# Optimization experiments

Hardware: AMD Instinct MI355X
Metric: run time of the kernel (lower is better)

Reference implementation:

```python
import jax, jax.numpy as jnp
import numpy as np

N = 100000       # nodes
E0 = 1600000     # random edges (self-loops appended -> E = E0 + N)
IN = 128         # input feature dim
H1, C1 = 8, 8    # conv1 heads, out channels per head
C2 = 64          # num_classes (conv2 out, heads=1)
NEG_SLOPE = 0.2


def gat_conv(x, src, dst, W, att_src, att_dst, bias, heads, out_ch, concat):
    """PyG-style GATConv (eval mode, no dropout). x: [N, F_in]."""
    n = x.shape[0]
    h = (x @ W).reshape(n, heads, out_ch)              # [N, H, C]
    a_src = jnp.sum(h * att_src, axis=-1)              # [N, H]
    a_dst = jnp.sum(h * att_dst, axis=-1)              # [N, H]
    e = jax.nn.leaky_relu(a_src[src] + a_dst[dst], NEG_SLOPE)  # [E, H]
    # segment softmax over edges grouped by destination node
    e_max = jax.ops.segment_max(e, dst, num_segments=n)
    ex = jnp.exp(e - e_max[dst])
    denom = jax.ops.segment_sum(ex, dst, num_segments=n)
    alpha = ex / denom[dst]                            # [E, H]
    msg = h[src] * alpha[:, :, None]                   # [E, H, C]
    out = jax.ops.segment_sum(msg, dst, num_segments=n)  # [N, H, C]
    out = out.reshape(n, heads * out_ch) if concat else out.mean(axis=1)
    return out + bias


def setup_inputs() -> dict:
    key = jax.random.key(0)
    ks = jax.random.split(key, 12)
    nodes = jnp.arange(N, dtype=jnp.int32)
    feat = jax.random.normal(ks[0], (N, IN), jnp.float32)
    src = jax.random.randint(ks[1], (E0,), 0, N, jnp.int32)
    dst = jax.random.randint(ks[2], (E0,), 0, N, jnp.int32)
    loop = jnp.arange(N, dtype=jnp.int32)
    edge_index = jnp.stack([jnp.concatenate([src, loop]),
                            jnp.concatenate([dst, loop])])  # [2, E]
    mask = jnp.ones((N,), bool)
    label = jax.random.randint(ks[3], (N,), 0, C2, jnp.int32)
    s = 0.1
    W1 = jax.random.normal(ks[4], (IN, H1 * C1), jnp.float32) * s
    att_src1 = jax.random.normal(ks[5], (H1, C1), jnp.float32) * s
    att_dst1 = jax.random.normal(ks[6], (H1, C1), jnp.float32) * s
    b1 = jnp.zeros((H1 * C1,), jnp.float32)
    W2 = jax.random.normal(ks[7], (H1 * C1, C2), jnp.float32) * s
    att_src2 = jax.random.normal(ks[8], (1, C2), jnp.float32) * s
    att_dst2 = jax.random.normal(ks[9], (1, C2), jnp.float32) * s
    b2 = jnp.zeros((C2,), jnp.float32)
    return {"nodes": nodes, "feat": feat, "edge_index": edge_index, "mask": mask,
            "label": label, "W1": W1, "att_src1": att_src1, "att_dst1": att_dst1,
            "b1": b1, "W2": W2, "att_src2": att_src2, "att_dst2": att_dst2, "b2": b2}


def reference(nodes, feat, edge_index, mask, label,
              W1, att_src1, att_dst1, b1, W2, att_src2, att_dst2, b2):
    src, dst = edge_index[0], edge_index[1]
    x = jax.nn.elu(gat_conv(feat, src, dst, W1, att_src1, att_dst1, b1,
                            H1, C1, concat=True))          # [N, 64]
    scores = gat_conv(x, src, dst, W2, att_src2, att_dst2, b2,
                      1, C2, concat=False)                  # [N, C2]
    logp = jax.nn.log_softmax(scores, axis=-1)
    nll = -jnp.take_along_axis(logp, label[:, None].astype(jnp.int32), axis=1)[:, 0]
    m = mask.astype(scores.dtype)
    loss = jnp.sum(nll * m) / jnp.sum(m)                    # masked mean CE
    pred = jnp.argmax(scores, axis=1)
    return loss, pred, label
```

## Files before the change

### kernel.cpp

```cpp
#include <hip/hip_runtime.h>
#include <cstdint>

#define NHEAD 8
#define D1 64
#define IN_F 128
#define NEG 0.2f
#define NBINS 256
#define BINS 1024
#define BSH 7
#define CHUNK 8192

__device__ __forceinline__ void fma4(float4& a, float s, const float4& v)
{
    a.x = fmaf(s, v.x, a.x); a.y = fmaf(s, v.y, a.y);
    a.z = fmaf(s, v.z, a.z); a.w = fmaf(s, v.w, a.w);
}

__global__ __launch_bounds__(256) void k_gemm1_hist(
    const float* __restrict__ feat,
    const float* __restrict__ W1,
    const float* __restrict__ att_s,
    const float* __restrict__ att_d,
    float* __restrict__ h1, float* __restrict__ a_src, float* __restrict__ a_dst,
    const int* __restrict__ dst, int* __restrict__ btot, int* __restrict__ bh,
    int N, int E, int GH)
{
    __shared__ float Wh[32 * 64];
    __shared__ float Fh[64 * 36];
    const int tid = threadIdx.x;

    if ((int)blockIdx.x < GH) {
        int* hist = (int*)Wh;
        for (int b = tid; b < BINS; b += 256) hist[b] = 0;
        __syncthreads();
        const int e0 = blockIdx.x * CHUNK;
        #pragma unroll
        for (int r = 0; r < 8; ++r) {
            int e = e0 + r * 1024 + tid * 4;
            if (e + 3 < E) {
                int4 d4 = *(const int4*)&dst[e];
                atomicAdd(&hist[d4.x >> BSH], 1);
                atomicAdd(&hist[d4.y >> BSH], 1);
                atomicAdd(&hist[d4.z >> BSH], 1);
                atomicAdd(&hist[d4.w >> BSH], 1);
            } else {
                for (int k = e; k < E && k < e + 4; ++k)
                    atomicAdd(&hist[dst[k] >> BSH], 1);
            }
        }
        __syncthreads();
        for (int b = tid; b < BINS; b += 256) {
            int c = hist[b];
            bh[(size_t)blockIdx.x * BINS + b] = c;
            if (c) atomicAdd(&btot[b * 16], c);
        }
        return;
    }

    const int tx = tid & 15, ty = tid >> 4;
    const int base = (blockIdx.x - GH) * 64;
    float4 acc0 = {0,0,0,0}, acc1 = {0,0,0,0}, acc2 = {0,0,0,0}, acc3 = {0,0,0,0};

    for (int p = 0; p < 4; ++p) {
        if (p) __syncthreads();
        for (int i = tid; i < 32 * 64; i += 256)
            Wh[i] = W1[p * 2048 + i];
        for (int i = tid; i < 64 * 32; i += 256) {
            int r = i >> 5, kk = i & 31;
            int n = base + r;
            Fh[r * 36 + kk] = (n < N) ? feat[(size_t)n * IN_F + p * 32 + kk] : 0.f;
        }
        __syncthreads();
        const float* wk = &Wh[4 * tx];
        const float* f0 = &Fh[(4 * ty + 0) * 36];
        const float* f1 = &Fh[(4 * ty + 1) * 36];
        const float* f2 = &Fh[(4 * ty + 2) * 36];
        const float* f3 = &Fh[(4 * ty + 3) * 36];
        #pragma unroll
        for (int kk = 0; kk < 32; kk += 4) {
            float4 fa = *(const float4*)&f0[kk];
            float4 fb = *(const float4*)&f1[kk];
            float4 fc = *(const float4*)&f2[kk];
            float4 fd = *(const float4*)&f3[kk];
            float4 w0 = *(const float4*)&wk[(kk + 0) * 64];
            float4 w1 = *(const float4*)&wk[(kk + 1) * 64];
            float4 w2 = *(const float4*)&wk[(kk + 2) * 64];
            float4 w3 = *(const float4*)&wk[(kk + 3) * 64];
            fma4(acc0, fa.x, w0); fma4(acc0, fa.y, w1); fma4(acc0, fa.z, w2); fma4(acc0, fa.w, w3);
            fma4(acc1, fb.x, w0); fma4(acc1, fb.y, w1); fma4(acc1, fb.z, w2); fma4(acc1, fb.w, w3);
            fma4(acc2, fc.x, w0); fma4(acc2, fc.y, w1); fma4(acc2, fc.z, w2); fma4(acc2, fc.w, w3);
            fma4(acc3, fd.x, w0); fma4(acc3, fd.y, w1); fma4(acc3, fd.z, w2); fma4(acc3, fd.w, w3);
        }
    }
    const float4 as4 = *(const float4*)&att_s[4 * tx];
    const float4 ad4 = *(const float4*)&att_d[4 * tx];
    float4 accs[4] = {acc0, acc1, acc2, acc3};
    #pragma unroll
    for (int i = 0; i < 4; ++i) {
        int n = base + 4 * ty + i;
        if (n < N) {
            *(float4*)&h1[(size_t)n * D1 + 4 * tx] = accs[i];
            float ps = accs[i].x * as4.x + accs[i].y * as4.y + accs[i].z * as4.z + accs[i].w * as4.w;
            float pd = accs[i].x * ad4.x + accs[i].y * ad4.y + accs[i].z * ad4.z + accs[i].w * ad4.w;
            ps += __shfl_xor(ps, 1);
            pd += __shfl_xor(pd, 1);
            if ((tx & 1) == 0) {
                a_src[n * NHEAD + (tx >> 1)] = ps;
                a_dst[n * NHEAD + (tx >> 1)] = pd;
            }
        }
    }
}

__device__ __forceinline__ int block_incl_scan(int v, int tid, int* lds4)
{
    int lane = tid & 63, w = tid >> 6;
    #pragma unroll
    for (int off = 1; off < 64; off <<= 1) {
        int t = __shfl_up(v, off);
        if (lane >= off) v += t;
    }
    if (lane == 63) lds4[w] = v;
    __syncthreads();
    int add = 0;
    #pragma unroll
    for (int i = 0; i < 4; ++i)
        if (i < w) add += lds4[i];
    __syncthreads();
    return v + add;
}

__global__ __launch_bounds__(256) void k_bscan(
    const int* __restrict__ btot, int* __restrict__ bbase, int* __restrict__ gcur,
    double* __restrict__ bins)
{
    __shared__ int lds4[4];
    const int tid = threadIdx.x;
    bins[tid] = 0.0;
    int c0 = btot[(4 * tid + 0) * 16];
    int c1 = btot[(4 * tid + 1) * 16];
    int c2 = btot[(4 * tid + 2) * 16];
    int c3 = btot[(4 * tid + 3) * 16];
    int v = c0 + c1 + c2 + c3;
    int incl = block_incl_scan(v, tid, lds4);
    int b0 = incl - v, b1 = b0 + c0, b2 = b1 + c1, b3 = b2 + c2;
    bbase[4 * tid + 0] = b0; gcur[(4 * tid + 0) * 16] = b0;
    bbase[4 * tid + 1] = b1; gcur[(4 * tid + 1) * 16] = b1;
    bbase[4 * tid + 2] = b2; gcur[(4 * tid + 2) * 16] = b2;
    bbase[4 * tid + 3] = b3; gcur[(4 * tid + 3) * 16] = b3;
}

__global__ __launch_bounds__(256) void k_scatter(
    const int* __restrict__ src, const int* __restrict__ dst,
    const int* __restrict__ bh, int* __restrict__ gcur,
    int* __restrict__ bucketed, int E)
{
    __shared__ int base[BINS], cur[BINS];
    const int tid = threadIdx.x;
    for (int b = tid; b < BINS; b += 256) {
        cur[b] = 0;
        int c = bh[(size_t)blockIdx.x * BINS + b];
        if (c) base[b] = atomicAdd(&gcur[b * 16], c);
    }
    __syncthreads();
    const int e0 = blockIdx.x * CHUNK;
    #pragma unroll
    for (int r = 0; r < 8; ++r) {
        int e = e0 + r * 1024 + tid * 4;
        if (e + 3 < E) {
            int4 d4 = *(const int4*)&dst[e];
            int4 s4 = *(const int4*)&src[e];
            int bx, rx;
            bx = d4.x >> BSH; rx = atomicAdd(&cur[bx], 1); bucketed[base[bx] + rx] = ((d4.x & 127) << 17) | s4.x;
            bx = d4.y >> BSH; rx = atomicAdd(&cur[bx], 1); bucketed[base[bx] + rx] = ((d4.y & 127) << 17) | s4.y;
            bx = d4.z >> BSH; rx = atomicAdd(&cur[bx], 1); bucketed[base[bx] + rx] = ((d4.z & 127) << 17) | s4.z;
            bx = d4.w >> BSH; rx = atomicAdd(&cur[bx], 1); bucketed[base[bx] + rx] = ((d4.w & 127) << 17) | s4.w;
        } else {
            for (int k = e; k < E && k < e + 4; ++k) {
                int d = dst[k];
                int bx = d >> BSH;
                int rx = atomicAdd(&cur[bx], 1);
                bucketed[base[bx] + rx] = ((d & 127) << 17) | src[k];
            }
        }
    }
}

__global__ __launch_bounds__(256) void k_seg(
    const int* __restrict__ btot, const int* __restrict__ bbase,
    const int* __restrict__ bucketed,
    int* __restrict__ deg, int* __restrict__ rowstart, int* __restrict__ srcs, int N)
{
    __shared__ int cnt[128], cur[128], lb[128];
    const int tid = threadIdx.x;
    const int b = blockIdx.x;
    const int gs = bbase[b];
    const int sz = btot[b * 16];
    if (tid < 128) { cnt[tid] = 0; cur[tid] = 0; }
    __syncthreads();
    for (int i = tid; i < sz; i += 256)
        atomicAdd(&cnt[bucketed[gs + i] >> 17], 1);
    __syncthreads();
    if (tid < 128) lb[tid] = cnt[tid];
    __syncthreads();
    #pragma unroll
    for (int off = 1; off < 128; off <<= 1) {
        int t = 0;
        if (tid < 128 && tid >= off) t = lb[tid - off];
        __syncthreads();
        if (tid < 128 && tid >= off) lb[tid] += t;
        __syncthreads();
    }
    if (tid < 128) {
        int ex = lb[tid] - cnt[tid];
        lb[tid] = ex;
        int d = b * 128 + tid;
        if (d < N) { deg[d] = cnt[tid]; rowstart[d] = gs + ex; }
    }
    __syncthreads();
    for (int i = tid; i < sz; i += 256) {
        int v = bucketed[gs + i];
        int d7 = v >> 17;
        int r = atomicAdd(&cur[d7], 1);
        srcs[gs + lb[d7] + r] = v & 0x1FFFF;
    }
}

__global__ __launch_bounds__(256) void k_agg1(
    const int* __restrict__ deg, const int* __restrict__ rowstart,
    const int* __restrict__ srcs,
    const float* __restrict__ a_s, const float* __restrict__ a_d,
    const float* __restrict__ h1, const float* __restrict__ b1,
    float* __restrict__ x, int N)
{
    const int tid = threadIdx.x, w = tid >> 6, j = tid & 63;
    const int t = j & 15, q = j >> 4;
    const int n = blockIdx.x * 4 + w;
    if (n >= N) return;
    const int rlen = deg[n];
    const int row = rowstart[n];
    const int h = t >> 1;
    const float ad = a_d[n * NHEAD + h];
    float4 acc = {0.f, 0.f, 0.f, 0.f};
    float den = 0.f;
    for (int base = 0; base < rlen; base += 16) {
        int mTot = rlen - base;
        if (4 * q < mTot) {
            int rem = mTot - 4 * q;
            int i0 = row + base + 4 * q;
            int s0 = srcs[i0];
            int s1 = rem > 1 ? srcs[i0 + 1] : 0;
            int s2 = rem > 2 ? srcs[i0 + 2] : 0;
            int s3 = rem > 3 ? srcs[i0 + 3] : 0;
            float v0 = a_s[s0 * NHEAD + h] + ad;
            float v1 = a_s[s1 * NHEAD + h] + ad;
            float v2 = a_s[s2 * NHEAD + h] + ad;
            float v3 = a_s[s3 * NHEAD + h] + ad;
            v0 = v0 > 0.f ? v0 : NEG * v0;
            v1 = v1 > 0.f ? v1 : NEG * v1;
            v2 = v2 > 0.f ? v2 : NEG * v2;
            v3 = v3 > 0.f ? v3 : NEG * v3;
            float e0 = __expf(v0);
            float e1 = rem > 1 ? __expf(v1) : 0.f;
            float e2 = rem > 2 ? __expf(v2) : 0.f;
            float e3 = rem > 3 ? __expf(v3) : 0.f;
            float4 l0 = *(const float4*)&h1[(size_t)s0 * D1 + 4 * t];
            float4 l1 = *(const float4*)&h1[(size_t)s1 * D1 + 4 * t];
            float4 l2 = *(const float4*)&h1[(size_t)s2 * D1 + 4 * t];
            float4 l3 = *(const float4*)&h1[(size_t)s3 * D1 + 4 * t];
            fma4(acc, e0, l0); fma4(acc, e1, l1);
            fma4(acc, e2, l2); fma4(acc, e3, l3);
            den += (e0 + e1) + (e2 + e3);
        }
    }
    acc.x += __shfl_xor(acc.x, 16); acc.y += __shfl_xor(acc.y, 16);
    acc.z += __shfl_xor(acc.z, 16); acc.w += __shfl_xor(acc.w, 16);
    den   += __shfl_xor(den, 16);
    acc.x += __shfl_xor(acc.x, 32); acc.y += __shfl_xor(acc.y, 32);
    acc.z += __shfl_xor(acc.z, 32); acc.w += __shfl_xor(acc.w, 32);
    den   += __shfl_xor(den, 32);
    if (q == 0) {
        float4 b = *(const float4*)&b1[4 * t];
        float4 o;
        o.x = acc.x / den + b.x; o.y = acc.y / den + b.y;
        o.z = acc.z / den + b.z; o.w = acc.w / den + b.w;
        o.x = o.x > 0.f ? o.x : expm1f(o.x);
        o.y = o.y > 0.f ? o.y : expm1f(o.y);
        o.z = o.z > 0.f ? o.z : expm1f(o.z);
        o.w = o.w > 0.f ? o.w : expm1f(o.w);
        *(float4*)&x[(size_t)n * D1 + 4 * t] = o;
    }
}

__global__ __launch_bounds__(256) void k_gemm2(
    const float* __restrict__ x,
    const float* __restrict__ W2,
    const float* __restrict__ att_s,
    const float* __restrict__ att_d,
    float* __restrict__ h2, float* __restrict__ a_src, float* __restrict__ a_dst,
    int N)
{
    __shared__ float Wh[64 * 64];
    __shared__ float Fh[64 * 68];
    const int tid = threadIdx.x;
    const int tx = tid & 15, ty = tid >> 4;
    const int base = blockIdx.x * 64;
    for (int i = tid; i < 64 * 64; i += 256)
        Wh[i] = W2[i];
    for (int i = tid; i < 64 * 64; i += 256) {
        int r = i >> 6, kk = i & 63;
        int n = base + r;
        Fh[r * 68 + kk] = (n < N) ? x[(size_t)n * 64 + kk] : 0.f;
    }
    __syncthreads();
    float4 acc0 = {0,0,0,0}, acc1 = {0,0,0,0}, acc2 = {0,0,0,0}, acc3 = {0,0,0,0};
    const float* wk = &Wh[4 * tx];
    const float* f0 = &Fh[(4 * ty + 0) * 68];
    const float* f1 = &Fh[(4 * ty + 1) * 68];
    const float* f2 = &Fh[(4 * ty + 2) * 68];
    const float* f3 = &Fh[(4 * ty + 3) * 68];
    #pragma unroll 4
    for (int kk = 0; kk < 64; kk += 4) {
        float4 fa = *(const float4*)&f0[kk];
        float4 fb = *(const float4*)&f1[kk];
        float4 fc = *(const float4*)&f2[kk];
        float4 fd = *(const float4*)&f3[kk];
        float4 w0 = *(const float4*)&wk[(kk + 0) * 64];
        float4 w1 = *(const float4*)&wk[(kk + 1) * 64];
        float4 w2 = *(const float4*)&wk[(kk + 2) * 64];
        float4 w3 = *(const float4*)&wk[(kk + 3) * 64];
        fma4(acc0, fa.x, w0); fma4(acc0, fa.y, w1); fma4(acc0, fa.z, w2); fma4(acc0, fa.w, w3);
        fma4(acc1, fb.x, w0); fma4(acc1, fb.y, w1); fma4(acc1, fb.z, w2); fma4(acc1, fb.w, w3);
        fma4(acc2, fc.x, w0); fma4(acc2, fc.y, w1); fma4(acc2, fc.z, w2); fma4(acc2, fc.w, w3);
        fma4(acc3, fd.x, w0); fma4(acc3, fd.y, w1); fma4(acc3, fd.z, w2); fma4(acc3, fd.w, w3);
    }
    const float4 as4 = *(const float4*)&att_s[4 * tx];
    const float4 ad4 = *(const float4*)&att_d[4 * tx];
    float4 accs[4] = {acc0, acc1, acc2, acc3};
    #pragma unroll
    for (int i = 0; i < 4; ++i) {
        int n = base + 4 * ty + i;
        if (n < N) {
            *(float4*)&h2[(size_t)n * 64 + 4 * tx] = accs[i];
            float ps = accs[i].x * as4.x + accs[i].y * as4.y + accs[i].z * as4.z + accs[i].w * as4.w;
            float pd = accs[i].x * ad4.x + accs[i].y * ad4.y + accs[i].z * ad4.z + accs[i].w * ad4.w;
            ps += __shfl_xor(ps, 1); pd += __shfl_xor(pd, 1);
            ps += __shfl_xor(ps, 2); pd += __shfl_xor(pd, 2);
            ps += __shfl_xor(ps, 4); pd += __shfl_xor(pd, 4);
            ps += __shfl_xor(ps, 8); pd += __shfl_xor(pd, 8);
            if (tx == 0) { a_src[n] = ps; a_dst[n] = pd; }
        }
    }
}

__global__ __launch_bounds__(256) void k_agg2(
    const int* __restrict__ deg, const int* __restrict__ rowstart,
    const int* __restrict__ srcs,
    const float* __restrict__ a_s, const float* __restrict__ a_d,
    const float* __restrict__ h2, const float* __restrict__ b2,
    const int* __restrict__ label,
    float* __restrict__ dout, double* __restrict__ bins, int N)
{
    __shared__ float snll[16];
    const int tid = threadIdx.x, j = tid & 63;
    const int t = j & 15, g16 = j & 0x30;
    const int n = blockIdx.x * 16 + (tid >> 4);
    if (tid < 16) snll[tid] = 0.f;
    __syncthreads();
    const bool valid = (n < N);
    const int rlen = valid ? deg[n] : 0;
    const int row  = valid ? rowstart[n] : 0;
    const float ad = valid ? a_d[n] : 0.f;
    float4 acc = {0.f, 0.f, 0.f, 0.f};
    float den = 0.f;
    for (int base = 0; base < rlen; base += 16) {
        int m = rlen - base; if (m > 16) m = 16;
        int myS = 0; float ex = 0.f;
        if (t < m) {
            myS = srcs[row + base + t];
            float v = a_s[myS] + ad;
            v = v > 0.f ? v : NEG * v;
            ex = __expf(v);
        }
        float ds = ex;
        ds += __shfl_xor(ds, 1); ds += __shfl_xor(ds, 2);
        ds += __shfl_xor(ds, 4); ds += __shfl_xor(ds, 8);
        den += ds;
        for (int kb = 0; kb < m; kb += 4) {
            int s0 = __shfl(myS, g16 | (kb + 0));
            int s1 = __shfl(myS, g16 | (kb + 1));
            int s2 = __shfl(myS, g16 | (kb + 2));
            int s3 = __shfl(myS, g16 | (kb + 3));
            float e0 = __shfl(ex, g16 | (kb + 0));
            float e1 = __shfl(ex, g16 | (kb + 1));
            float e2 = __shfl(ex, g16 | (kb + 2));
            float e3 = __shfl(ex, g16 | (kb + 3));
            float4 l0 = *(const float4*)&h2[(size_t)s0 * 64 + 4 * t];
            float4 l1 = *(const float4*)&h2[(size_t)s1 * 64 + 4 * t];
            float4 l2 = *(const float4*)&h2[(size_t)s2 * 64 + 4 * t];
            float4 l3 = *(const float4*)&h2[(size_t)s3 * 64 + 4 * t];
            fma4(acc, e0, l0);
            fma4(acc, e1, l1);
            fma4(acc, e2, l2);
            fma4(acc, e3, l3);
        }
    }
    float4 b = *(const float4*)&b2[4 * t];
    float4 sc;
    sc.x = acc.x / den + b.x; sc.y = acc.y / den + b.y;
    sc.z = acc.z / den + b.z; sc.w = acc.w / den + b.w;
    float mv = sc.x; int mi = 4 * t;
    if (sc.y > mv) { mv = sc.y; mi = 4 * t + 1; }
    if (sc.z > mv) { mv = sc.z; mi = 4 * t + 2; }
    if (sc.w > mv) { mv = sc.w; mi = 4 * t + 3; }
    #pragma unroll
    for (int off = 1; off < 16; off <<= 1) {
        float ov = __shfl_xor(mv, off);
        int oi = __shfl_xor(mi, off);
        if (ov > mv || (ov == mv && oi < mi)) { mv = ov; mi = oi; }
    }
    float se = __expf(sc.x - mv) + __expf(sc.y - mv) + __expf(sc.z - mv) + __expf(sc.w - mv);
    #pragma unroll
    for (int off = 1; off < 16; off <<= 1) se += __shfl_xor(se, off);
    int lab = valid ? label[n] : 0;
    int comp = lab & 3;
    float cl = comp == 0 ? sc.x : comp == 1 ? sc.y : comp == 2 ? sc.z : sc.w;
    float sl = __shfl(cl, g16 | (lab >> 2));
    if (t == 0 && valid) {
        snll[tid >> 4] = mv + logf(se) - sl;
        dout[1 + n] = (float)mi;
        dout[1 + (size_t)N + n] = (float)lab;
    }
    __syncthreads();
    if (tid == 0) {
        double bs = 0.0;
        #pragma unroll
        for (int i = 0; i < 16; ++i) bs += (double)snll[i];
        atomicAdd(&bins[blockIdx.x & (NBINS - 1)], bs);
    }
}

__global__ __launch_bounds__(256) void k_loss(
    const double* __restrict__ bins, float* __restrict__ dout, int N)
{
    __shared__ double sw[4];
    const int tid = threadIdx.x;
    double v = bins[tid];
    #pragma unroll
    for (int off = 1; off < 64; off <<= 1) v += __shfl_xor(v, off);
    if ((tid & 63) == 0) sw[tid >> 6] = v;
    __syncthreads();
    if (tid == 0)
        dout[0] = (float)((sw[0] + sw[1] + sw[2] + sw[3]) / (double)N);
}

extern "C" void kernel_launch(void* const* d_in, const int* in_sizes, int n_in,
                              void* d_out, int out_size, void* d_ws, size_t ws_size,
                              hipStream_t stream)
{
    const float* feat   = (const float*)d_in[1];
    const int*   edge   = (const int*)d_in[2];
    const int*   label  = (const int*)d_in[4];
    const float* W1     = (const float*)d_in[5];
    const float* att_s1 = (const float*)d_in[6];
    const float* att_d1 = (const float*)d_in[7];
    const float* b1     = (const float*)d_in[8];
    const float* W2     = (const float*)d_in[9];
    const float* att_s2 = (const float*)d_in[10];
    const float* att_d2 = (const float*)d_in[11];
    const float* b2     = (const float*)d_in[12];

    const int N = in_sizes[0];
    const int E = in_sizes[2] / 2;
    const int* src = edge;
    const int* dst = edge + E;

    float* bufA = (float*)d_ws;
    float* bufB = bufA + (size_t)N * 64;
    float* a_s1 = bufB + (size_t)N * 64;
    float* a_d1 = a_s1 + (size_t)N * 8;
    int*   deg  = (int*)(a_d1 + (size_t)N * 8);
    int*   rowstart = deg + N;
    int*   srcs = rowstart + N;
    double* bins = (double*)(((uintptr_t)(srcs + E) + 7) & ~(uintptr_t)7);

    int* bucketed = (int*)bufB;
    int* btot  = bucketed + E;
    int* gcur  = btot + BINS * 16;
    int* bbase = gcur + BINS * 16;
    int* bh    = bbase + BINS;

    float* a_s2 = a_s1;
    float* a_d2 = a_s1 + N;

    float* out = (float*)d_out;

    const int GH    = (E + CHUNK - 1) / CHUNK;
    const int G1    = (N + 63) / 64;
    const int NBUCK = (N + 127) / 128;

    hipMemsetAsync(btot, 0, (size_t)BINS * 16 * sizeof(int), stream);

    k_gemm1_hist<<<GH + G1, 256, 0, stream>>>(feat, W1, att_s1, att_d1,
                                              bufA, a_s1, a_d1,
                                              dst, btot, bh, N, E, GH);
    k_bscan  <<<1, 256, 0, stream>>>(btot, bbase, gcur, bins);
    k_scatter<<<GH, 256, 0, stream>>>(src, dst, bh, gcur, bucketed, E);
    k_seg    <<<NBUCK, 256, 0, stream>>>(btot, bbase, bucketed, deg, rowstart, srcs, N);

    k_agg1 <<<(N + 3) / 4, 256, 0, stream>>>(deg, rowstart, srcs, a_s1, a_d1,
                                             bufA, b1, bufB, N);
    k_gemm2<<<G1, 256, 0, stream>>>(bufB, W2, att_s2, att_d2, bufA, a_s2, a_d2, N);
    k_agg2 <<<(N + 15) / 16, 256, 0, stream>>>(deg, rowstart, srcs, a_s2, a_d2,
                                               bufA, b2, label, out, bins, N);
    k_loss <<<1, 256, 0, stream>>>(bins, out, N);
}
```

Measured before the change: 389.6 us.

## Fuse layer-1 aggregation with layer-2 GEMM and fold loss into agg2

Merges the conv1 aggregation kernel with the conv2 projection: each wave aggregates one node, writes the ELU output to shared memory, multiplies it by W2 held in LDS, and computes the attention scalars. The kernel becomes a persistent grid-stride loop over 2048 blocks. The separate loss kernel is removed; the last agg2 block, found through an atomic counter, performs the final reduction. This removes the x round trip through global memory and two launches, at the cost of a per-node 64x64 matvec in LDS and an intra-wave sync that relies on waitcnt instead of a barrier.

```diff
diff --git a/kernel.cpp b/kernel.cpp
--- a/kernel.cpp
+++ b/kernel.cpp
@@ -132,11 +132,12 @@
 
 __global__ __launch_bounds__(256) void k_bscan(
     const int* __restrict__ btot, int* __restrict__ bbase, int* __restrict__ gcur,
-    double* __restrict__ bins)
+    double* __restrict__ bins, int* __restrict__ lcnt)
 {
     __shared__ int lds4[4];
     const int tid = threadIdx.x;
     bins[tid] = 0.0;
+    if (tid == 0) lcnt[0] = 0;
     int c0 = btot[(4 * tid + 0) * 16];
     int c1 = btot[(4 * tid + 1) * 16];
     int c2 = btot[(4 * tid + 2) * 16];
@@ -226,129 +227,97 @@
     }
 }
 
-__global__ __launch_bounds__(256) void k_agg1(
+__global__ __launch_bounds__(256) void k_agg1f(
     const int* __restrict__ deg, const int* __restrict__ rowstart,
     const int* __restrict__ srcs,
     const float* __restrict__ a_s, const float* __restrict__ a_d,
     const float* __restrict__ h1, const float* __restrict__ b1,
-    float* __restrict__ x, int N)
-{
+    const float* __restrict__ W2,
+    const float* __restrict__ att_s2, const float* __restrict__ att_d2,
+    float* __restrict__ h2, float* __restrict__ a_s2, float* __restrict__ a_d2,
+    int N)
+{
+    __shared__ float W2s[64 * 64];
+    __shared__ float xrow[4][64];
+    __shared__ float h2row[4][64];
     const int tid = threadIdx.x, w = tid >> 6, j = tid & 63;
     const int t = j & 15, q = j >> 4;
-    const int n = blockIdx.x * 4 + w;
-    if (n >= N) return;
-    const int rlen = deg[n];
-    const int row = rowstart[n];
     const int h = t >> 1;
-    const float ad = a_d[n * NHEAD + h];
-    float4 acc = {0.f, 0.f, 0.f, 0.f};
-    float den = 0.f;
-    for (int base = 0; base < rlen; base += 16) {
-        int mTot = rlen - base;
-        if (4 * q < mTot) {
-            int rem = mTot - 4 * q;
-            int i0 = row + base + 4 * q;
-            int s0 = srcs[i0];
-            int s1 = rem > 1 ? srcs[i0 + 1] : 0;
-            int s2 = rem > 2 ? srcs[i0 + 2] : 0;
-            int s3 = rem > 3 ? srcs[i0 + 3] : 0;
-            float v0 = a_s[s0 * NHEAD + h] + ad;
-            float v1 = a_s[s1 * NHEAD + h] + ad;
-            float v2 = a_s[s2 * NHEAD + h] + ad;
-            float v3 = a_s[s3 * NHEAD + h] + ad;
-            v0 = v0 > 0.f ? v0 : NEG * v0;
-            v1 = v1 > 0.f ? v1 : NEG * v1;
-            v2 = v2 > 0.f ? v2 : NEG * v2;
-            v3 = v3 > 0.f ? v3 : NEG * v3;
-            float e0 = __expf(v0);
-            float e1 = rem > 1 ? __expf(v1) : 0.f;
-            float e2 = rem > 2 ? __expf(v2) : 0.f;
-            float e3 = rem > 3 ? __expf(v3) : 0.f;
-            float4 l0 = *(const float4*)&h1[(size_t)s0 * D1 + 4 * t];
-            float4 l1 = *(const float4*)&h1[(size_t)s1 * D1 + 4 * t];
-            float4 l2 = *(const float4*)&h1[(size_t)s2 * D1 + 4 * t];
-            float4 l3 = *(const float4*)&h1[(size_t)s3 * D1 + 4 * t];
-            fma4(acc, e0, l0); fma4(acc, e1, l1);
-            fma4(acc, e2, l2); fma4(acc, e3, l3);
-            den += (e0 + e1) + (e2 + e3);
-        }
-    }
-    acc.x += __shfl_xor(acc.x, 16); acc.y += __shfl_xor(acc.y, 16);
-    acc.z += __shfl_xor(acc.z, 16); acc.w += __shfl_xor(acc.w, 16);
-    den   += __shfl_xor(den, 16);
-    acc.x += __shfl_xor(acc.x, 32); acc.y += __shfl_xor(acc.y, 32);
-    acc.z += __shfl_xor(acc.z, 32); acc.w += __shfl_xor(acc.w, 32);
-    den   += __shfl_xor(den, 32);
-    if (q == 0) {
-        float4 b = *(const float4*)&b1[4 * t];
-        float4 o;
-        o.x = acc.x / den + b.x; o.y = acc.y / den + b.y;
-        o.z = acc.z / den + b.z; o.w = acc.w / den + b.w;
-        o.x = o.x > 0.f ? o.x : expm1f(o.x);
-        o.y = o.y > 0.f ? o.y : expm1f(o.y);
-        o.z = o.z > 0.f ? o.z : expm1f(o.z);
-        o.w = o.w > 0.f ? o.w : expm1f(o.w);
-        *(float4*)&x[(size_t)n * D1 + 4 * t] = o;
-    }
-}
-
-__global__ __launch_bounds__(256) void k_gemm2(
-    const float* __restrict__ x,
-    const float* __restrict__ W2,
-    const float* __restrict__ att_s,
-    const float* __restrict__ att_d,
-    float* __restrict__ h2, float* __restrict__ a_src, float* __restrict__ a_dst,
-    int N)
-{
-    __shared__ float Wh[64 * 64];
-    __shared__ float Fh[64 * 68];
-    const int tid = threadIdx.x;
-    const int tx = tid & 15, ty = tid >> 4;
-    const int base = blockIdx.x * 64;
-    for (int i = tid; i < 64 * 64; i += 256)
-        Wh[i] = W2[i];
-    for (int i = tid; i < 64 * 64; i += 256) {
-        int r = i >> 6, kk = i & 63;
-        int n = base + r;
-        Fh[r * 68 + kk] = (n < N) ? x[(size_t)n * 64 + kk] : 0.f;
-    }
-    __syncthreads();
-    float4 acc0 = {0,0,0,0}, acc1 = {0,0,0,0}, acc2 = {0,0,0,0}, acc3 = {0,0,0,0};
-    const float* wk = &Wh[4 * tx];
-    const float* f0 = &Fh[(4 * ty + 0) * 68];
-    const float* f1 = &Fh[(4 * ty + 1) * 68];
-    const float* f2 = &Fh[(4 * ty + 2) * 68];
-    const float* f3 = &Fh[(4 * ty + 3) * 68];
-    #pragma unroll 4
-    for (int kk = 0; kk < 64; kk += 4) {
-        float4 fa = *(const float4*)&f0[kk];
-        float4 fb = *(const float4*)&f1[kk];
-        float4 fc = *(const float4*)&f2[kk];
-        float4 fd = *(const float4*)&f3[kk];
-        float4 w0 = *(const float4*)&wk[(kk + 0) * 64];
-        float4 w1 = *(const float4*)&wk[(kk + 1) * 64];
-        float4 w2 = *(const float4*)&wk[(kk + 2) * 64];
-        float4 w3 = *(const float4*)&wk[(kk + 3) * 64];
-        fma4(acc0, fa.x, w0); fma4(acc0, fa.y, w1); fma4(acc0, fa.z, w2); fma4(acc0, fa.w, w3);
-        fma4(acc1, fb.x, w0); fma4(acc1, fb.y, w1); fma4(acc1, fb.z, w2); fma4(acc1, fb.w, w3);
-        fma4(acc2, fc.x, w0); fma4(acc2, fc.y, w1); fma4(acc2, fc.z, w2); fma4(acc2, fc.w, w3);
-        fma4(acc3, fd.x, w0); fma4(acc3, fd.y, w1); fma4(acc3, fd.z, w2); fma4(acc3, fd.w, w3);
-    }
-    const float4 as4 = *(const float4*)&att_s[4 * tx];
-    const float4 ad4 = *(const float4*)&att_d[4 * tx];
-    float4 accs[4] = {acc0, acc1, acc2, acc3};
-    #pragma unroll
-    for (int i = 0; i < 4; ++i) {
-        int n = base + 4 * ty + i;
-        if (n < N) {
-            *(float4*)&h2[(size_t)n * 64 + 4 * tx] = accs[i];
-            float ps = accs[i].x * as4.x + accs[i].y * as4.y + accs[i].z * as4.z + accs[i].w * as4.w;
-            float pd = accs[i].x * ad4.x + accs[i].y * ad4.y + accs[i].z * ad4.z + accs[i].w * ad4.w;
+    for (int i = tid; i < 64 * 64; i += 256) W2s[i] = W2[i];
+    __syncthreads();
+    const float4 bb  = *(const float4*)&b1[4 * t];
+    const float4 as4 = *(const float4*)&att_s2[4 * t];
+    const float4 ad4 = *(const float4*)&att_d2[4 * t];
+
+    for (int n = blockIdx.x * 4 + w; n < N; n += gridDim.x * 4) {
+        const int rlen = deg[n];
+        const int row = rowstart[n];
+        const float ad = a_d[n * NHEAD + h];
+        float4 acc = {0.f, 0.f, 0.f, 0.f};
+        float den = 0.f;
+        for (int base = 0; base < rlen; base += 16) {
+            int mTot = rlen - base;
+            if (4 * q < mTot) {
+                int rem = mTot - 4 * q;
+                int i0 = row + base + 4 * q;
+                int s0 = srcs[i0];
+                int s1 = rem > 1 ? srcs[i0 + 1] : 0;
+                int s2 = rem > 2 ? srcs[i0 + 2] : 0;
+                int s3 = rem > 3 ? srcs[i0 + 3] : 0;
+                float v0 = a_s[s0 * NHEAD + h] + ad;
+                float v1 = a_s[s1 * NHEAD + h] + ad;
+                float v2 = a_s[s2 * NHEAD + h] + ad;
+                float v3 = a_s[s3 * NHEAD + h] + ad;
+                v0 = v0 > 0.f ? v0 : NEG * v0;
+                v1 = v1 > 0.f ? v1 : NEG * v1;
+                v2 = v2 > 0.f ? v2 : NEG * v2;
+                v3 = v3 > 0.f ? v3 : NEG * v3;
+                float e0 = __expf(v0);
+                float e1 = rem > 1 ? __expf(v1) : 0.f;
+                float e2 = rem > 2 ? __expf(v2) : 0.f;
+                float e3 = rem > 3 ? __expf(v3) : 0.f;
+                float4 l0 = *(const float4*)&h1[(size_t)s0 * D1 + 4 * t];
+                float4 l1 = *(const float4*)&h1[(size_t)s1 * D1 + 4 * t];
+                float4 l2 = *(const float4*)&h1[(size_t)s2 * D1 + 4 * t];
+                float4 l3 = *(const float4*)&h1[(size_t)s3 * D1 + 4 * t];
+                fma4(acc, e0, l0); fma4(acc, e1, l1);
+                fma4(acc, e2, l2); fma4(acc, e3, l3);
+                den += (e0 + e1) + (e2 + e3);
+            }
+        }
+        acc.x += __shfl_xor(acc.x, 16); acc.y += __shfl_xor(acc.y, 16);
+        acc.z += __shfl_xor(acc.z, 16); acc.w += __shfl_xor(acc.w, 16);
+        den   += __shfl_xor(den, 16);
+        acc.x += __shfl_xor(acc.x, 32); acc.y += __shfl_xor(acc.y, 32);
+        acc.z += __shfl_xor(acc.z, 32); acc.w += __shfl_xor(acc.w, 32);
+        den   += __shfl_xor(den, 32);
+        if (q == 0) {
+            float4 o;
+            o.x = acc.x / den + bb.x; o.y = acc.y / den + bb.y;
+            o.z = acc.z / den + bb.z; o.w = acc.w / den + bb.w;
+            o.x = o.x > 0.f ? o.x : expm1f(o.x);
+            o.y = o.y > 0.f ? o.y : expm1f(o.y);
+            o.z = o.z > 0.f ? o.z : expm1f(o.z);
+            o.w = o.w > 0.f ? o.w : expm1f(o.w);
+            *(float4*)&xrow[w][4 * t] = o;
+        }
+        asm volatile("s_waitcnt lgkmcnt(0)" ::: "memory");
+        float hj = 0.f;
+        #pragma unroll 16
+        for (int k = 0; k < 64; ++k)
+            hj = fmaf(xrow[w][k], W2s[k * 64 + j], hj);
+        h2row[w][j] = hj;
+        asm volatile("s_waitcnt lgkmcnt(0)" ::: "memory");
+        if (q == 0) {
+            float4 hv = *(const float4*)&h2row[w][4 * t];
+            *(float4*)&h2[(size_t)n * 64 + 4 * t] = hv;
+            float ps = hv.x * as4.x + hv.y * as4.y + hv.z * as4.z + hv.w * as4.w;
+            float pd = hv.x * ad4.x + hv.y * ad4.y + hv.z * ad4.z + hv.w * ad4.w;
             ps += __shfl_xor(ps, 1); pd += __shfl_xor(pd, 1);
             ps += __shfl_xor(ps, 2); pd += __shfl_xor(pd, 2);
             ps += __shfl_xor(ps, 4); pd += __shfl_xor(pd, 4);
             ps += __shfl_xor(ps, 8); pd += __shfl_xor(pd, 8);
-            if (tx == 0) { a_src[n] = ps; a_dst[n] = pd; }
+            if (t == 0) { a_s2[n] = ps; a_d2[n] = pd; }
         }
     }
 }
@@ -359,9 +328,12 @@
     const float* __restrict__ a_s, const float* __restrict__ a_d,
     const float* __restrict__ h2, const float* __restrict__ b2,
     const int* __restrict__ label,
-    float* __restrict__ dout, double* __restrict__ bins, int N)
+    float* __restrict__ dout, double* __restrict__ bins, int* __restrict__ lcnt,
+    int N)
 {
     __shared__ float snll[16];
+    __shared__ int lastFlag;
+    __shared__ double sw[4];
     const int tid = threadIdx.x, j = tid & 63;
     const int t = j & 15, g16 = j & 0x30;
     const int n = blockIdx.x * 16 + (tid >> 4);
@@ -437,21 +409,19 @@
         #pragma unroll
         for (int i = 0; i < 16; ++i) bs += (double)snll[i];
         atomicAdd(&bins[blockIdx.x & (NBINS - 1)], bs);
-    }
-}
-
-__global__ __launch_bounds__(256) void k_loss(
-    const double* __restrict__ bins, float* __restrict__ dout, int N)
-{
-    __shared__ double sw[4];
-    const int tid = threadIdx.x;
-    double v = bins[tid];
-    #pragma unroll
-    for (int off = 1; off < 64; off <<= 1) v += __shfl_xor(v, off);
-    if ((tid & 63) == 0) sw[tid >> 6] = v;
-    __syncthreads();
-    if (tid == 0)
-        dout[0] = (float)((sw[0] + sw[1] + sw[2] + sw[3]) / (double)N);
+        __threadfence();
+        lastFlag = (atomicAdd(lcnt, 1) == (int)gridDim.x - 1);
+    }
+    __syncthreads();
+    if (lastFlag) {
+        double v = atomicAdd(&bins[tid], 0.0);
+        #pragma unroll
+        for (int off = 1; off < 64; off <<= 1) v += __shfl_xor(v, off);
+        if ((tid & 63) == 0) sw[tid >> 6] = v;
+        __syncthreads();
+        if (tid == 0)
+            dout[0] = (float)((sw[0] + sw[1] + sw[2] + sw[3]) / (double)N);
+    }
 }
 
 extern "C" void kernel_launch(void* const* d_in, const int* in_sizes, int n_in,
@@ -483,6 +453,9 @@
     int*   rowstart = deg + N;
     int*   srcs = rowstart + N;
     double* bins = (double*)(((uintptr_t)(srcs + E) + 7) & ~(uintptr_t)7);
+    int*   lcnt = (int*)(bins + NBINS);
+    float* a_s2 = (float*)(lcnt + 4);
+    float* a_d2 = a_s2 + N;
 
     int* bucketed = (int*)bufB;
     int* btot  = bucketed + E;
@@ -490,9 +463,6 @@
     int* bbase = gcur + BINS * 16;
     int* bh    = bbase + BINS;
 
-    float* a_s2 = a_s1;
-    float* a_d2 = a_s1 + N;
-
     float* out = (float*)d_out;
 
     const int GH    = (E + CHUNK - 1) / CHUNK;
@@ -504,14 +474,13 @@
     k_gemm1_hist<<<GH + G1, 256, 0, stream>>>(feat, W1, att_s1, att_d1,
                                               bufA, a_s1, a_d1,
                                               dst, btot, bh, N, E, GH);
-    k_bscan  <<<1, 256, 0, stream>>>(btot, bbase, gcur, bins);
+    k_bscan  <<<1, 256, 0, stream>>>(btot, bbase, gcur, bins, lcnt);
     k_scatter<<<GH, 256, 0, stream>>>(src, dst, bh, gcur, bucketed, E);
     k_seg    <<<NBUCK, 256, 0, stream>>>(btot, bbase, bucketed, deg, rowstart, srcs, N);
 
-    k_agg1 <<<(N + 3) / 4, 256, 0, stream>>>(deg, rowstart, srcs, a_s1, a_d1,
-                                             bufA, b1, bufB, N);
-    k_gemm2<<<G1, 256, 0, stream>>>(bufB, W2, att_s2, att_d2, bufA, a_s2, a_d2, N);
+    k_agg1f<<<2048, 256, 0, stream>>>(deg, rowstart, srcs, a_s1, a_d1,
+                                      bufA, b1, W2, att_s2, att_d2,
+                                      bufB, a_s2, a_d2, N);
     k_agg2 <<<(N + 15) / 16, 256, 0, stream>>>(deg, rowstart, srcs, a_s2, a_d2,
-                                               bufA, b2, label, out, bins, N);
-    k_loss <<<1, 256, 0, stream>>>(bins, out, N);
-}
+                                               bufB, b2, label, out, bins, lcnt, N);
+}
```

After: 595.4 us. +52.8%, slower.
